# Optimization experiments

Hardware: AMD Instinct MI355X
Metric: run time of the kernel (lower is better)

Reference implementation:

```python
import jax, jax.numpy as jnp
import numpy as np

D_MODEL = 1024
H = 16
D_HEAD = D_MODEL // H
MASK_VAL = -1e30


def setup_inputs() -> dict:
    key = jax.random.key(0)
    ks = jax.random.split(key, 10)
    B, S = 2, 2048
    scale = 1.0 / np.sqrt(D_MODEL)
    return {
        "query": jax.random.normal(ks[0], (B, S, D_MODEL), jnp.float32),
        "key": jax.random.normal(ks[1], (B, S, D_MODEL), jnp.float32),
        "value": jax.random.normal(ks[2], (B, S, D_MODEL), jnp.float32),
        "mask": jax.random.randint(ks[3], (B, S, S), 0, 2) > 0,
        "Wq": jax.random.normal(ks[4], (D_MODEL, D_MODEL), jnp.float32) * scale,
        "bq": jnp.zeros((D_MODEL,), jnp.float32),
        "Wk": jax.random.normal(ks[5], (D_MODEL, D_MODEL), jnp.float32) * scale,
        "bk": jnp.zeros((D_MODEL,), jnp.float32),
        "Wv": jax.random.normal(ks[6], (D_MODEL, D_MODEL), jnp.float32) * scale,
        "bv": jnp.zeros((D_MODEL,), jnp.float32),
    }


def _split_heads(x, B, S):
    # [B,S,D] -> [B,H,S,Dh]
    return x.reshape(B, S, H, D_HEAD).transpose(0, 2, 1, 3)


def reference(query, key, value, mask, Wq, bq, Wk, bk, Wv, bv):
    B, S, _ = query.shape
    q = _split_heads(query @ Wq.T + bq, B, S)
    k = _split_heads(key @ Wk.T + bk, B, S)
    v = _split_heads(value @ Wv.T + bv, B, S)
    # scale by sqrt of per-head dim (query.size(-1) after split)
    q = q / jnp.sqrt(jnp.asarray(D_HEAD, q.dtype))
    scores = jnp.einsum("bhqd,bhkd->bhqk", q, k)
    scores = jnp.where(mask[:, None, :, :], MASK_VAL, scores)
    attn = jax.nn.softmax(scores, axis=-1)
    out = jnp.einsum("bhqk,bhkd->bhqd", attn, v)
    return out.transpose(0, 2, 1, 3).reshape(B, S, D_MODEL)
```

## Files before the change

### kernel.cpp

```cpp
#include <hip/hip_runtime.h>
#include <hip/hip_bf16.h>

#define D_MODEL 1024
#define NH 16
#define DH 64
#define S_LEN 2048
#define BATCH 2
#define QSCALE (0.125f * 1.44269504088896f)

#define KV_HSTRIDE (S_LEN * DH)
#define WS_V_OFF   (NH * KV_HSTRIDE)
#define KVB_WORDS  (2 * NH * KV_HSTRIDE)
#define MB_WORDS   ((S_LEN / 64) * S_LEN)
#define KTILE 128
#define NT (S_LEN / KTILE)
#define X_ELEMS (BATCH * S_LEN * D_MODEL)
#define W_ELEMS (D_MODEL * D_MODEL)
#define KSTR 88
#define VSTR 136
#define BUFW (128 * KSTR + 64 * VSTR)
#define BUF_BYTES (BUFW * 2)

typedef __attribute__((ext_vector_type(8))) short bf16x8;
typedef __attribute__((ext_vector_type(4))) float f32x4;
typedef __attribute__((ext_vector_type(2))) unsigned int u32x2;

static __device__ inline unsigned short f2bf(float f) {
    union { float f; unsigned u; } v; v.f = f;
    unsigned r = v.u + 0x7fffu + ((v.u >> 16) & 1u);
    return (unsigned short)(r >> 16);
}
static __device__ inline unsigned cvt2(float a, float b) {
    union { __hip_bfloat162 h2; unsigned u; } cv;
    cv.h2 = __float22bfloat162_rn(make_float2(a, b));
    return cv.u;
}
static __device__ inline bf16x8 pack8(f32x4 a, f32x4 b) {
    union { bf16x8 v; unsigned u[4]; } r;
    r.u[0] = cvt2(a[0], a[1]); r.u[1] = cvt2(a[2], a[3]);
    r.u[2] = cvt2(b[0], b[1]); r.u[3] = cvt2(b[2], b[3]);
    return r.v;
}
static __device__ inline bf16x8 cvt8(const float* __restrict__ p) {
    return pack8(*(const f32x4*)p, *(const f32x4*)(p + 4));
}
static __device__ inline float exp2_fast(float x) {
#if __has_builtin(__builtin_amdgcn_exp2f)
    return __builtin_amdgcn_exp2f(x);
#else
    return exp2f(x);
#endif
}
static __device__ inline void gload_lds16(const unsigned short* __restrict__ g,
                                          unsigned short* l, int lane) {
#if __has_builtin(__builtin_amdgcn_global_load_lds)
    __builtin_amdgcn_global_load_lds(
        (const __attribute__((address_space(1))) void*)g,
        (__attribute__((address_space(3))) void*)l, 16, 0, 0);
#else
    *(bf16x8*)((char*)l + lane * 16) = *(const bf16x8*)g;
#endif
}
static __device__ inline int vperm(int s) {
    return (s & ~31) | ((s & 12) << 1) | ((s & 16) >> 2) | (s & 3);
}

__global__ __launch_bounds__(256) void cvt_kernel(
    const float* __restrict__ q, const float* __restrict__ k,
    const float* __restrict__ v,
    const float* __restrict__ Wq, const float* __restrict__ Wk,
    const float* __restrict__ Wv,
    unsigned short* __restrict__ xb, unsigned short* __restrict__ wb)
{
    const int by = blockIdx.y;
    const float* src;
    unsigned short* dst;
    size_t base;
    if (blockIdx.x < 1024) {
        src = by == 0 ? q : (by == 1 ? k : v);
        dst = xb + (size_t)by * X_ELEMS;
        base = (size_t)blockIdx.x * 4096;
    } else {
        src = by == 0 ? Wq : (by == 1 ? Wk : Wv);
        dst = wb + (size_t)by * W_ELEMS;
        base = (size_t)(blockIdx.x - 1024) * 4096;
    }
    const int tid = threadIdx.x;
#pragma unroll
    for (int j = 0; j < 4; ++j) {
        const size_t o = base + (size_t)j * 1024 + (size_t)tid * 4;
        const f32x4 a = *(const f32x4*)(src + o);
        u32x2 r;
        r[0] = cvt2(a[0], a[1]);
        r[1] = cvt2(a[2], a[3]);
        *(u32x2*)&dst[o] = r;
    }
}

__global__ __launch_bounds__(256) void pack_mask_kernel(
    const int* __restrict__ mask, unsigned long long* __restrict__ mbits,
    int b_base)
{
    const int w    = blockIdx.x * 4 + (threadIdx.x >> 6);
    const int lane = threadIdx.x & 63;
    const int b    = b_base + (w >> 16);
    const int rem  = w & 65535;
    const int kt   = rem >> 11;
    const int s    = rem & 2047;
    const int v = mask[((size_t)b * S_LEN + s) * S_LEN + kt * 64 + lane];
    const unsigned long long bits = __ballot(v != 0);
    if (lane == 0) mbits[w] = bits;
}

__global__ __launch_bounds__(256) void proj_v2_kernel(
    const unsigned short* __restrict__ xb, const unsigned short* __restrict__ wb,
    const float* __restrict__ bq, const float* __restrict__ bk,
    const float* __restrict__ bv,
    float* __restrict__ q_out, unsigned short* __restrict__ ws)
{
    const int bx = blockIdx.x;
    const int by = blockIdx.y;
    const int z  = by >> 3;
    const int c0 = (by & 7) * 128;

    const unsigned short* A  = xb + (size_t)z * X_ELEMS;
    const unsigned short* Bw = wb + (size_t)z * W_ELEMS;
    const float* bias = z == 0 ? bq : (z == 1 ? bk : bv);

    const int tid  = threadIdx.x;
    const int wave = tid >> 6;
    const int lane = tid & 63;
    const int quad = lane >> 4;
    const int l16  = lane & 15;
    const int m0   = (wave & 1) * 64;
    const int n0   = (wave >> 1) * 64;

    __shared__ __align__(16) unsigned short As[128 * 32];
    __shared__ __align__(16) unsigned short Bs[128 * 32];

    const int r_lo = wave * 16 + (lane >> 2);
    const int r_hi = (wave + 4) * 16 + (lane >> 2);
    const int segu = (lane & 3) * 8;
    const int row0 = bx * 128;

    f32x4 acc[4][4] = {};

    for (int kk = 0; kk < D_MODEL; kk += 32) {
        gload_lds16(A  + (size_t)(row0 + r_lo) * D_MODEL + kk + segu, &As[wave * 512], lane);
        gload_lds16(A  + (size_t)(row0 + r_hi) * D_MODEL + kk + segu, &As[(wave + 4) * 512], lane);
        gload_lds16(Bw + (size_t)(c0 + r_lo) * D_MODEL + kk + segu, &Bs[wave * 512], lane);
        gload_lds16(Bw + (size_t)(c0 + r_hi) * D_MODEL + kk + segu, &Bs[(wave + 4) * 512], lane);
        __syncthreads();

        bf16x8 af[4], bfr[4];
#pragma unroll
        for (int i = 0; i < 4; ++i)
            af[i] = *(const bf16x8*)&As[(m0 + i * 16 + l16) * 32 + quad * 8];
#pragma unroll
        for (int j = 0; j < 4; ++j)
            bfr[j] = *(const bf16x8*)&Bs[(n0 + j * 16 + l16) * 32 + quad * 8];
#pragma unroll
        for (int i = 0; i < 4; ++i)
#pragma unroll
            for (int j = 0; j < 4; ++j)
                acc[i][j] = __builtin_amdgcn_mfma_f32_16x16x32_bf16(
                    af[i], bfr[j], acc[i][j], 0, 0, 0);
        __syncthreads();
    }

#pragma unroll
    for (int j = 0; j < 4; ++j) {
        const int cl  = c0 + n0 + j * 16 + l16;
        const float bval = bias[cl];
        const int h  = cl >> 6;
        const int dh = cl & 63;
#pragma unroll
        for (int i = 0; i < 4; ++i) {
#pragma unroll
            for (int r = 0; r < 4; ++r) {
                const int row = row0 + m0 + i * 16 + quad * 4 + r;
                const float v = acc[i][j][r] + bval;
                if (z == 0) {
                    q_out[(size_t)row * D_MODEL + cl] = v * QSCALE;
                } else {
                    unsigned short* slab = ws + (size_t)(row >> 11) * KVB_WORDS;
                    const int s = row & 2047;
                    if (z == 1)
                        slab[(size_t)h * KV_HSTRIDE + s * DH + dh] = f2bf(v);
                    else
                        slab[WS_V_OFF + (size_t)h * KV_HSTRIDE + dh * S_LEN + vperm(s)] = f2bf(v);
                }
            }
        }
    }
}

__global__ __launch_bounds__(256) void proj_fb_kernel(
    const float* __restrict__ q_in, const float* __restrict__ k_in,
    const float* __restrict__ v_in,
    const float* __restrict__ Wq, const float* __restrict__ bq,
    const float* __restrict__ Wk, const float* __restrict__ bk,
    const float* __restrict__ Wv, const float* __restrict__ bv,
    float* __restrict__ q_out, unsigned short* __restrict__ ws, int b_base)
{
    const int bx = blockIdx.x;
    const int by = blockIdx.y;
    const int z  = by >> 3;
    const int c0 = (by & 7) * 128;

    const float* x    = z == 0 ? q_in : (z == 1 ? k_in : v_in);
    const float* W    = z == 0 ? Wq   : (z == 1 ? Wk   : Wv);
    const float* bias = z == 0 ? bq   : (z == 1 ? bk   : bv);

    const int tid  = threadIdx.x;
    const int wave = tid >> 6;
    const int lane = tid & 63;
    const int quad = lane >> 4;
    const int l16  = lane & 15;
    const int m0   = (wave & 1) * 64;
    const int n0   = (wave >> 1) * 64;

    __shared__ __align__(16) unsigned short As[128][40];
    __shared__ __align__(16) unsigned short Bs[128][40];

    const int srow = tid >> 1;
    const int kcol = (tid & 1) * 16;
    const int row0 = b_base * S_LEN + bx * 128;
    const float* ag = x + (size_t)(row0 + srow) * D_MODEL + kcol;
    const float* bg = W + (size_t)(c0 + srow) * D_MODEL + kcol;

    f32x4 acc[4][4] = {};

    for (int kk = 0; kk < D_MODEL; kk += 32) {
        {
            f32x4 a0 = *(const f32x4*)(ag + kk);
            f32x4 a1 = *(const f32x4*)(ag + kk + 4);
            f32x4 a2 = *(const f32x4*)(ag + kk + 8);
            f32x4 a3 = *(const f32x4*)(ag + kk + 12);
            f32x4 b0 = *(const f32x4*)(bg + kk);
            f32x4 b1 = *(const f32x4*)(bg + kk + 4);
            f32x4 b2 = *(const f32x4*)(bg + kk + 8);
            f32x4 b3 = *(const f32x4*)(bg + kk + 12);
            *(bf16x8*)&As[srow][kcol]     = pack8(a0, a1);
            *(bf16x8*)&As[srow][kcol + 8] = pack8(a2, a3);
            *(bf16x8*)&Bs[srow][kcol]     = pack8(b0, b1);
            *(bf16x8*)&Bs[srow][kcol + 8] = pack8(b2, b3);
        }
        __syncthreads();

        bf16x8 af[4], bfr[4];
#pragma unroll
        for (int i = 0; i < 4; ++i)
            af[i] = *(const bf16x8*)&As[m0 + i * 16 + l16][quad * 8];
#pragma unroll
        for (int j = 0; j < 4; ++j)
            bfr[j] = *(const bf16x8*)&Bs[n0 + j * 16 + l16][quad * 8];
#pragma unroll
        for (int i = 0; i < 4; ++i)
#pragma unroll
            for (int j = 0; j < 4; ++j)
                acc[i][j] = __builtin_amdgcn_mfma_f32_16x16x32_bf16(
                    af[i], bfr[j], acc[i][j], 0, 0, 0);
        __syncthreads();
    }

#pragma unroll
    for (int j = 0; j < 4; ++j) {
        const int cl  = c0 + n0 + j * 16 + l16;
        const float bval = bias[cl];
        const int h  = cl >> 6;
        const int dh = cl & 63;
#pragma unroll
        for (int i = 0; i < 4; ++i) {
#pragma unroll
            for (int r = 0; r < 4; ++r) {
                const int row = row0 + m0 + i * 16 + quad * 4 + r;
                const float v = acc[i][j][r] + bval;
                if (z == 0) {
                    q_out[(size_t)row * D_MODEL + cl] = v * QSCALE;
                } else {
                    const int b_rel = (row >> 11) - b_base;
                    const int s     = row & 2047;
                    unsigned short* slab = ws + (size_t)b_rel * KVB_WORDS;
                    if (z == 1)
                        slab[(size_t)h * KV_HSTRIDE + s * DH + dh] = f2bf(v);
                    else
                        slab[WS_V_OFF + (size_t)h * KV_HSTRIDE + dh * S_LEN + vperm(s)] = f2bf(v);
                }
            }
        }
    }
}

__global__ __launch_bounds__(256) void attn_db_kernel(
    const unsigned short* __restrict__ ws,
    const unsigned long long* __restrict__ mbits,
    float* __restrict__ out)
{
    const int h     = blockIdx.x;
    const int qtile = blockIdx.y;
    const int bz    = blockIdx.z;

    const unsigned short* K  = ws + (size_t)bz * KVB_WORDS + (size_t)h * KV_HSTRIDE;
    const unsigned short* Vg = K + WS_V_OFF;
    const unsigned long long* mb = mbits + (size_t)bz * MB_WORDS;

    const int tid  = threadIdx.x;
    const int wave = tid >> 6;
    const int lane = tid & 63;
    const int quad = lane >> 4;
    const int l16  = lane & 15;
    const int q0   = qtile * 128;

    extern __shared__ __align__(16) unsigned short lds[];

    bf16x8 aq0a, aq1a, aq0b, aq1b;
    {
        const float* qa =
            out + (size_t)(bz * S_LEN + q0 + wave * 16 + l16) * D_MODEL + h * DH;
        const float* qb = qa + (size_t)64 * D_MODEL;
        aq0a = cvt8(qa + quad * 8);  aq1a = cvt8(qa + 32 + quad * 8);
        aq0b = cvt8(qb + quad * 8);  aq1b = cvt8(qb + 32 + quad * 8);
    }

    bf16x8 ones;
    {
        union { bf16x8 v; unsigned short u[8]; } o;
#pragma unroll
        for (int i = 0; i < 8; ++i) o.u[i] = 0x3F80;
        ones = o.v;
    }

    const int qg = q0 + wave * 16 + l16;
    f32x4 l_acc_a = {0.f, 0.f, 0.f, 0.f};
    f32x4 l_acc_b = {0.f, 0.f, 0.f, 0.f};
    f32x4 o_a[4] = {}, o_b[4] = {};

    const int krow = tid >> 1, kc = (tid & 1) * 32;
    const int vrow = tid >> 2, vc = (tid & 3) * 32;
    bf16x8 kr[4], vr[4];
    {
        const unsigned short* kp = K + (size_t)krow * DH + kc;
        const unsigned short* vp = Vg + (size_t)vrow * S_LEN + vc;
#pragma unroll
        for (int i = 0; i < 4; ++i) {
            kr[i] = *(const bf16x8*)(kp + 8 * i);
            vr[i] = *(const bf16x8*)(vp + 8 * i);
        }
    }
    unsigned long long wm0a = mb[qg] >> (quad * 4);
    unsigned long long wm1a = mb[(size_t)S_LEN + qg] >> (quad * 4);
    unsigned long long wm0b = mb[qg + 64] >> (quad * 4);
    unsigned long long wm1b = mb[(size_t)S_LEN + qg + 64] >> (quad * 4);

    {
        unsigned short* Kt0 = lds;
        unsigned short* Vt0 = lds + 128 * KSTR;
#pragma unroll
        for (int i = 0; i < 4; ++i) {
            *(bf16x8*)&Kt0[krow * KSTR + kc + 8 * i] = kr[i];
            *(bf16x8*)&Vt0[vrow * VSTR + vc + 8 * i] = vr[i];
        }
    }

    for (int kt = 0; kt < NT; ++kt) {
        __syncthreads();
        unsigned short* Ktc = lds + (kt & 1) * BUFW;
        unsigned short* Vtc = Ktc + 128 * KSTR;

        if (kt + 1 < NT) {
            const unsigned short* kp = K + (size_t)((kt + 1) * KTILE + krow) * DH + kc;
            const unsigned short* vp = Vg + (size_t)vrow * S_LEN + (kt + 1) * KTILE + vc;
#pragma unroll
            for (int i = 0; i < 4; ++i) {
                kr[i] = *(const bf16x8*)(kp + 8 * i);
                vr[i] = *(const bf16x8*)(vp + 8 * i);
            }
        }
        unsigned long long nm0a = 0ull, nm1a = 0ull, nm0b = 0ull, nm1b = 0ull;
        if (kt + 1 < NT) {
            nm0a = mb[(size_t)(2 * kt + 2) * S_LEN + qg] >> (quad * 4);
            nm1a = mb[(size_t)(2 * kt + 3) * S_LEN + qg] >> (quad * 4);
            nm0b = mb[(size_t)(2 * kt + 2) * S_LEN + qg + 64] >> (quad * 4);
            nm1b = mb[(size_t)(2 * kt + 3) * S_LEN + qg + 64] >> (quad * 4);
        }

        bf16x8 af_a[4], af_b[4];
#pragma unroll
        for (int c = 0; c < 4; ++c) {
            f32x4 sa[2], sb[2];
            __builtin_amdgcn_s_setprio(1);
#pragma unroll
            for (int j = 0; j < 2; ++j) {
                const int blk = 2 * c + j;
                const unsigned short* kb = &Ktc[(blk * 16 + l16) * KSTR];
                bf16x8 k0 = *(const bf16x8*)&kb[quad * 8];
                bf16x8 k1 = *(const bf16x8*)&kb[32 + quad * 8];
                f32x4 z = {0.f, 0.f, 0.f, 0.f};
                sa[j] = __builtin_amdgcn_mfma_f32_16x16x32_bf16(k0, aq0a, z, 0, 0, 0);
                sa[j] = __builtin_amdgcn_mfma_f32_16x16x32_bf16(k1, aq1a, sa[j], 0, 0, 0);
                sb[j] = __builtin_amdgcn_mfma_f32_16x16x32_bf16(k0, aq0b, z, 0, 0, 0);
                sb[j] = __builtin_amdgcn_mfma_f32_16x16x32_bf16(k1, aq1b, sb[j], 0, 0, 0);
            }
            __builtin_amdgcn_s_setprio(0);
#pragma unroll
            for (int j = 0; j < 2; ++j) {
                const int blk = 2 * c + j;
                const unsigned long long wa = (blk < 4) ? wm0a : wm1a;
                const unsigned long long wb = (blk < 4) ? wm0b : wm1b;
                const int sh = (blk & 3) * 16;
#pragma unroll
                for (int r = 0; r < 4; ++r) {
                    const bool ma  = (wa >> (sh + r)) & 1ull;
                    const bool mbk = (wb >> (sh + r)) & 1ull;
                    sa[j][r] = ma  ? 0.0f : exp2_fast(sa[j][r]);
                    sb[j][r] = mbk ? 0.0f : exp2_fast(sb[j][r]);
                }
            }
            {
                union { bf16x8 v; unsigned u[4]; } pk;
                pk.u[0] = cvt2(sa[0][0], sa[0][1]);
                pk.u[1] = cvt2(sa[0][2], sa[0][3]);
                pk.u[2] = cvt2(sa[1][0], sa[1][1]);
                pk.u[3] = cvt2(sa[1][2], sa[1][3]);
                af_a[c] = pk.v;
                pk.u[0] = cvt2(sb[0][0], sb[0][1]);
                pk.u[1] = cvt2(sb[0][2], sb[0][3]);
                pk.u[2] = cvt2(sb[1][0], sb[1][1]);
                pk.u[3] = cvt2(sb[1][2], sb[1][3]);
                af_b[c] = pk.v;
            }
        }

        __builtin_amdgcn_s_setprio(1);
#pragma unroll
        for (int c = 0; c < 4; ++c) {
            l_acc_a = __builtin_amdgcn_mfma_f32_16x16x32_bf16(af_a[c], ones, l_acc_a, 0, 0, 0);
            l_acc_b = __builtin_amdgcn_mfma_f32_16x16x32_bf16(af_b[c], ones, l_acc_b, 0, 0, 0);
        }
#pragma unroll
        for (int d = 0; d < 4; ++d) {
#pragma unroll
            for (int c = 0; c < 4; ++c) {
                bf16x8 bv = *(const bf16x8*)&Vtc[(d * 16 + l16) * VSTR + c * 32 + quad * 8];
                o_a[d] = __builtin_amdgcn_mfma_f32_16x16x32_bf16(af_a[c], bv, o_a[d], 0, 0, 0);
                o_b[d] = __builtin_amdgcn_mfma_f32_16x16x32_bf16(af_b[c], bv, o_b[d], 0, 0, 0);
            }
        }
        __builtin_amdgcn_s_setprio(0);

        if (kt + 1 < NT) {
            unsigned short* Ktn = lds + ((kt + 1) & 1) * BUFW;
            unsigned short* Vtn = Ktn + 128 * KSTR;
#pragma unroll
            for (int i = 0; i < 4; ++i) {
                *(bf16x8*)&Ktn[krow * KSTR + kc + 8 * i] = kr[i];
                *(bf16x8*)&Vtn[vrow * VSTR + vc + 8 * i] = vr[i];
            }
        }
        wm0a = nm0a; wm1a = nm1a; wm0b = nm0b; wm1b = nm1b;
    }

#pragma unroll
    for (int r = 0; r < 4; ++r) {
        const float ia = 1.0f / fmaxf(l_acc_a[r], 1e-30f);
        const float ib = 1.0f / fmaxf(l_acc_b[r], 1e-30f);
        const int qgr = q0 + wave * 16 + quad * 4 + r;
#pragma unroll
        for (int d = 0; d < 4; ++d) {
            out[((size_t)(bz * S_LEN) + qgr) * D_MODEL + h * DH + d * 16 + l16] =
                o_a[d][r] * ia;
            out[((size_t)(bz * S_LEN) + qgr + 64) * D_MODEL + h * DH + d * 16 + l16] =
                o_b[d][r] * ib;
        }
    }
}

__global__ __launch_bounds__(256) void attn_sb_kernel(
    const unsigned short* __restrict__ ws,
    const unsigned long long* __restrict__ mbits,
    const int* __restrict__ mask,
    float* __restrict__ out, int b_base, int use_bits)
{
    const int h     = blockIdx.x;
    const int qtile = blockIdx.y;
    const int bz    = blockIdx.z;
    const int b0    = b_base + bz;

    const unsigned short* K  = ws + (size_t)bz * KVB_WORDS + (size_t)h * KV_HSTRIDE;
    const unsigned short* Vg = K + WS_V_OFF;
    const unsigned long long* mb = mbits + (size_t)bz * MB_WORDS;

    const int tid  = threadIdx.x;
    const int wave = tid >> 6;
    const int lane = tid & 63;
    const int quad = lane >> 4;
    const int l16  = lane & 15;
    const int q0   = qtile * 128;

    __shared__ __align__(16) unsigned short Vt[64][VSTR];
    __shared__ __align__(16) unsigned short Kt[128 * KSTR];

    bf16x8 aq0a, aq1a, aq0b, aq1b;
    {
        const float* qa =
            out + (size_t)(b0 * S_LEN + q0 + wave * 16 + l16) * D_MODEL + h * DH;
        const float* qb = qa + (size_t)64 * D_MODEL;
        aq0a = cvt8(qa + quad * 8);  aq1a = cvt8(qa + 32 + quad * 8);
        aq0b = cvt8(qb + quad * 8);  aq1b = cvt8(qb + 32 + quad * 8);
    }

    const int qg = q0 + wave * 16 + l16;
    float l_a = 0.f, l_b = 0.f;
    f32x4 o_a[4] = {}, o_b[4] = {};

    const int krow = tid >> 1, kc = (tid & 1) * 32;
    const int vrow = tid >> 2, vc = (tid & 3) * 32;
    bf16x8 kr[4], vr[4];
    {
        const unsigned short* kp = K + (size_t)krow * DH + kc;
        const unsigned short* vp = Vg + (size_t)vrow * S_LEN + vc;
#pragma unroll
        for (int i = 0; i < 4; ++i) {
            kr[i] = *(const bf16x8*)(kp + 8 * i);
            vr[i] = *(const bf16x8*)(vp + 8 * i);
        }
    }

    for (int kt = 0; kt < NT; ++kt) {
#pragma unroll
        for (int i = 0; i < 4; ++i) {
            *(bf16x8*)&Kt[krow * KSTR + kc + 8 * i] = kr[i];
            *(bf16x8*)&Vt[vrow][vc + 8 * i]         = vr[i];
        }
        __syncthreads();

        if (kt + 1 < NT) {
            const unsigned short* kp = K + (size_t)((kt + 1) * KTILE + krow) * DH + kc;
            const unsigned short* vp = Vg + (size_t)vrow * S_LEN + (kt + 1) * KTILE + vc;
#pragma unroll
            for (int i = 0; i < 4; ++i) {
                kr[i] = *(const bf16x8*)(kp + 8 * i);
                vr[i] = *(const bf16x8*)(vp + 8 * i);
            }
        }

        unsigned long long wm0a = 0ull, wm1a = 0ull, wm0b = 0ull, wm1b = 0ull;
        if (use_bits) {
            wm0a = mb[(size_t)(2 * kt) * S_LEN + qg] >> (quad * 4);
            wm1a = mb[(size_t)(2 * kt + 1) * S_LEN + qg] >> (quad * 4);
            wm0b = mb[(size_t)(2 * kt) * S_LEN + qg + 64] >> (quad * 4);
            wm1b = mb[(size_t)(2 * kt + 1) * S_LEN + qg + 64] >> (quad * 4);
        }

        bf16x8 af_a[4], af_b[4];
#pragma unroll
        for (int c = 0; c < 4; ++c) {
            f32x4 sa[2], sb[2];
#pragma unroll
            for (int j = 0; j < 2; ++j) {
                const int blk = 2 * c + j;
                const unsigned short* kb = &Kt[(blk * 16 + l16) * KSTR];
                bf16x8 k0 = *(const bf16x8*)&kb[quad * 8];
                bf16x8 k1 = *(const bf16x8*)&kb[32 + quad * 8];
                f32x4 z = {0.f, 0.f, 0.f, 0.f};
                sa[j] = __builtin_amdgcn_mfma_f32_16x16x32_bf16(k0, aq0a, z, 0, 0, 0);
                sa[j] = __builtin_amdgcn_mfma_f32_16x16x32_bf16(k1, aq1a, sa[j], 0, 0, 0);
                sb[j] = __builtin_amdgcn_mfma_f32_16x16x32_bf16(k0, aq0b, z, 0, 0, 0);
                sb[j] = __builtin_amdgcn_mfma_f32_16x16x32_bf16(k1, aq1b, sb[j], 0, 0, 0);
            }
#pragma unroll
            for (int j = 0; j < 2; ++j) {
                const int blk = 2 * c + j;
                const unsigned long long wa = (blk < 4) ? wm0a : wm1a;
                const unsigned long long wb = (blk < 4) ? wm0b : wm1b;
                const int sh = (blk & 3) * 16;
#pragma unroll
                for (int r = 0; r < 4; ++r) {
                    bool ma, mbk;
                    if (use_bits) {
                        ma  = (wa >> (sh + r)) & 1ull;
                        mbk = (wb >> (sh + r)) & 1ull;
                    } else {
                        const int kg = kt * KTILE + blk * 16 + quad * 4 + r;
                        ma  = mask[((size_t)(b0 * S_LEN) + qg) * S_LEN + kg] != 0;
                        mbk = mask[((size_t)(b0 * S_LEN) + qg + 64) * S_LEN + kg] != 0;
                    }
                    const float pa = ma  ? 0.0f : exp2_fast(sa[j][r]);
                    const float pb = mbk ? 0.0f : exp2_fast(sb[j][r]);
                    sa[j][r] = pa; l_a += pa;
                    sb[j][r] = pb; l_b += pb;
                }
            }
            {
                union { bf16x8 v; unsigned u[4]; } pk;
                pk.u[0] = cvt2(sa[0][0], sa[0][1]);
                pk.u[1] = cvt2(sa[0][2], sa[0][3]);
                pk.u[2] = cvt2(sa[1][0], sa[1][1]);
                pk.u[3] = cvt2(sa[1][2], sa[1][3]);
                af_a[c] = pk.v;
                pk.u[0] = cvt2(sb[0][0], sb[0][1]);
                pk.u[1] = cvt2(sb[0][2], sb[0][3]);
                pk.u[2] = cvt2(sb[1][0], sb[1][1]);
                pk.u[3] = cvt2(sb[1][2], sb[1][3]);
                af_b[c] = pk.v;
            }
        }

#pragma unroll
        for (int d = 0; d < 4; ++d) {
#pragma unroll
            for (int c = 0; c < 4; ++c) {
                bf16x8 bv = *(const bf16x8*)&Vt[d * 16 + l16][c * 32 + quad * 8];
                o_a[d] = __builtin_amdgcn_mfma_f32_16x16x32_bf16(af_a[c], bv, o_a[d], 0, 0, 0);
                o_b[d] = __builtin_amdgcn_mfma_f32_16x16x32_bf16(af_b[c], bv, o_b[d], 0, 0, 0);
            }
        }
        __syncthreads();
    }

    l_a += __shfl_xor(l_a, 16, 64);
    l_a += __shfl_xor(l_a, 32, 64);
    l_b += __shfl_xor(l_b, 16, 64);
    l_b += __shfl_xor(l_b, 32, 64);

#pragma unroll
    for (int r = 0; r < 4; ++r) {
        const float la = __shfl(l_a, quad * 4 + r, 64);
        const float lb = __shfl(l_b, quad * 4 + r, 64);
        const float ia = 1.0f / fmaxf(la, 1e-30f);
        const float ib = 1.0f / fmaxf(lb, 1e-30f);
        const int qgr = q0 + wave * 16 + quad * 4 + r;
#pragma unroll
        for (int d = 0; d < 4; ++d) {
            out[((size_t)(b0 * S_LEN) + qgr) * D_MODEL + h * DH + d * 16 + l16] =
                o_a[d][r] * ia;
            out[((size_t)(b0 * S_LEN) + qgr + 64) * D_MODEL + h * DH + d * 16 + l16] =
                o_b[d][r] * ib;
        }
    }
}

extern "C" void kernel_launch(void* const* d_in, const int* in_sizes, int n_in,
                              void* d_out, int out_size, void* d_ws, size_t ws_size,
                              hipStream_t stream) {
    const float* query = (const float*)d_in[0];
    const float* key   = (const float*)d_in[1];
    const float* value = (const float*)d_in[2];
    const int*   mask  = (const int*)d_in[3];
    const float* Wq    = (const float*)d_in[4];
    const float* bq    = (const float*)d_in[5];
    const float* Wk    = (const float*)d_in[6];
    const float* bk    = (const float*)d_in[7];
    const float* Wv    = (const float*)d_in[8];
    const float* bv    = (const float*)d_in[9];

    unsigned short* ws   = (unsigned short*)d_ws;
    float*          outp = (float*)d_out;

    const size_t KV_BYTES = (size_t)KVB_WORDS * 2;
    const size_t MB_BYTES = (size_t)MB_WORDS * 8;
    const size_t XB_BYTES = (size_t)3 * X_ELEMS * 2;
    const size_t WB_BYTES = (size_t)3 * W_ELEMS * 2;
    const size_t base2    = 2 * KV_BYTES + 2 * MB_BYTES;

    static int db_ok = -1;
    if (db_ok < 0) {
        hipError_t e = hipFuncSetAttribute(
            reinterpret_cast<const void*>(attn_db_kernel),
            hipFuncAttributeMaxDynamicSharedMemorySize, 2 * BUF_BYTES);
        db_ok = (e == hipSuccess) ? 1 : 0;
    }

    if (ws_size >= base2 + XB_BYTES + WB_BYTES) {
        unsigned long long* mbits = (unsigned long long*)(ws + 2 * KVB_WORDS);
        unsigned short* xb = ws + base2 / 2;
        unsigned short* wb = xb + (size_t)3 * X_ELEMS;
        cvt_kernel<<<dim3(1280, 3), 256, 0, stream>>>(
            query, key, value, Wq, Wk, Wv, xb, wb);
        proj_v2_kernel<<<dim3(32, 24), 256, 0, stream>>>(
            xb, wb, bq, bk, bv, outp, ws);
        pack_mask_kernel<<<dim3(2 * MB_WORDS / 4), 256, 0, stream>>>(mask, mbits, 0);
        if (db_ok)
            attn_db_kernel<<<dim3(NH, S_LEN / 128, 2), 256, 2 * BUF_BYTES, stream>>>(
                ws, mbits, outp);
        else
            attn_sb_kernel<<<dim3(NH, S_LEN / 128, 2), 256, 0, stream>>>(
                ws, mbits, mask, outp, 0, 1);
    } else if (ws_size >= base2) {
        unsigned long long* mbits = (unsigned long long*)(ws + 2 * KVB_WORDS);
        proj_fb_kernel<<<dim3(32, 24), 256, 0, stream>>>(
            query, key, value, Wq, bq, Wk, bk, Wv, bv, outp, ws, 0);
        pack_mask_kernel<<<dim3(2 * MB_WORDS / 4), 256, 0, stream>>>(mask, mbits, 0);
        if (db_ok)
            attn_db_kernel<<<dim3(NH, S_LEN / 128, 2), 256, 2 * BUF_BYTES, stream>>>(
                ws, mbits, outp);
        else
            attn_sb_kernel<<<dim3(NH, S_LEN / 128, 2), 256, 0, stream>>>(
                ws, mbits, mask, outp, 0, 1);
    } else if (ws_size >= KV_BYTES + MB_BYTES) {
        unsigned long long* mbits = (unsigned long long*)(ws + KVB_WORDS);
        for (int b0 = 0; b0 < BATCH; ++b0) {
            proj_fb_kernel<<<dim3(16, 24), 256, 0, stream>>>(
                query, key, value, Wq, bq, Wk, bk, Wv, bv, outp, ws, b0);
            pack_mask_kernel<<<dim3(MB_WORDS / 4), 256, 0, stream>>>(mask, mbits, b0);
            attn_sb_kernel<<<dim3(NH, S_LEN / 128, 1), 256, 0, stream>>>(
                ws, mbits, mask, outp, b0, 1);
        }
    } else {
        for (int b0 = 0; b0 < BATCH; ++b0) {
            proj_fb_kernel<<<dim3(16, 24), 256, 0, stream>>>(
                query, key, value, Wq, bq, Wk, bk, Wv, bv, outp, ws, b0);
            attn_sb_kernel<<<dim3(NH, S_LEN / 128, 1), 256, 0, stream>>>(
                ws, (const unsigned long long*)ws, mask, outp, b0, 0);
        }
    }
}
```

Before: 252.6 us.

## Load V fragments directly from global memory and sum softmax denominators on VALU

The attention kernel stops staging V tiles in shared memory. Each wave now reads its V MFMA operands straight from global memory (the transposed V layout), and only K is double-buffered in static LDS. The row-sum of probabilities is accumulated with scalar adds plus cross-lane shuffles instead of extra MFMAs against a ones vector, and the dynamic-LDS attribute setup is removed. This shrinks LDS use and LDS traffic and may raise occupancy. The cost is that every wave redundantly fetches the same V data from global/L2, and the V loads sit on the critical path with less latency hiding.

```diff
diff --git a/kernel.cpp b/kernel.cpp
--- a/kernel.cpp
+++ b/kernel.cpp
@@ -18,8 +18,6 @@
 #define W_ELEMS (D_MODEL * D_MODEL)
 #define KSTR 88
 #define VSTR 136
-#define BUFW (128 * KSTR + 64 * VSTR)
-#define BUF_BYTES (BUFW * 2)
 
 typedef __attribute__((ext_vector_type(8))) short bf16x8;
 typedef __attribute__((ext_vector_type(4))) float f32x4;
@@ -312,7 +310,7 @@
     const int l16  = lane & 15;
     const int q0   = qtile * 128;
 
-    extern __shared__ __align__(16) unsigned short lds[];
+    __shared__ __align__(16) unsigned short Kt[2][128 * KSTR];
 
     bf16x8 aq0a, aq1a, aq0b, aq1b;
     {
@@ -323,59 +321,43 @@
         aq0b = cvt8(qb + quad * 8);  aq1b = cvt8(qb + 32 + quad * 8);
     }
 
-    bf16x8 ones;
-    {
-        union { bf16x8 v; unsigned short u[8]; } o;
-#pragma unroll
-        for (int i = 0; i < 8; ++i) o.u[i] = 0x3F80;
-        ones = o.v;
-    }
-
     const int qg = q0 + wave * 16 + l16;
-    f32x4 l_acc_a = {0.f, 0.f, 0.f, 0.f};
-    f32x4 l_acc_b = {0.f, 0.f, 0.f, 0.f};
+    float l_a = 0.f, l_b = 0.f;
     f32x4 o_a[4] = {}, o_b[4] = {};
 
     const int krow = tid >> 1, kc = (tid & 1) * 32;
-    const int vrow = tid >> 2, vc = (tid & 3) * 32;
-    bf16x8 kr[4], vr[4];
+    bf16x8 kr[4];
     {
         const unsigned short* kp = K + (size_t)krow * DH + kc;
-        const unsigned short* vp = Vg + (size_t)vrow * S_LEN + vc;
-#pragma unroll
-        for (int i = 0; i < 4; ++i) {
-            kr[i] = *(const bf16x8*)(kp + 8 * i);
-            vr[i] = *(const bf16x8*)(vp + 8 * i);
-        }
-    }
+#pragma unroll
+        for (int i = 0; i < 4; ++i) kr[i] = *(const bf16x8*)(kp + 8 * i);
+    }
+    const unsigned short* vbase = Vg + (size_t)l16 * S_LEN + quad * 8;
+
     unsigned long long wm0a = mb[qg] >> (quad * 4);
     unsigned long long wm1a = mb[(size_t)S_LEN + qg] >> (quad * 4);
     unsigned long long wm0b = mb[qg + 64] >> (quad * 4);
     unsigned long long wm1b = mb[(size_t)S_LEN + qg + 64] >> (quad * 4);
 
-    {
-        unsigned short* Kt0 = lds;
-        unsigned short* Vt0 = lds + 128 * KSTR;
-#pragma unroll
-        for (int i = 0; i < 4; ++i) {
-            *(bf16x8*)&Kt0[krow * KSTR + kc + 8 * i] = kr[i];
-            *(bf16x8*)&Vt0[vrow * VSTR + vc + 8 * i] = vr[i];
-        }
-    }
+#pragma unroll
+    for (int i = 0; i < 4; ++i)
+        *(bf16x8*)&Kt[0][krow * KSTR + kc + 8 * i] = kr[i];
 
     for (int kt = 0; kt < NT; ++kt) {
         __syncthreads();
-        unsigned short* Ktc = lds + (kt & 1) * BUFW;
-        unsigned short* Vtc = Ktc + 128 * KSTR;
+        const unsigned short* Ktc = Kt[kt & 1];
+        const unsigned short* vcol = vbase + kt * KTILE;
 
         if (kt + 1 < NT) {
             const unsigned short* kp = K + (size_t)((kt + 1) * KTILE + krow) * DH + kc;
-            const unsigned short* vp = Vg + (size_t)vrow * S_LEN + (kt + 1) * KTILE + vc;
-#pragma unroll
-            for (int i = 0; i < 4; ++i) {
-                kr[i] = *(const bf16x8*)(kp + 8 * i);
-                vr[i] = *(const bf16x8*)(vp + 8 * i);
-            }
+#pragma unroll
+            for (int i = 0; i < 4; ++i) kr[i] = *(const bf16x8*)(kp + 8 * i);
+        }
+        bf16x8 vA0[4], vA1[4];
+#pragma unroll
+        for (int c = 0; c < 4; ++c) {
+            vA0[c] = *(const bf16x8*)(vcol + c * 32);
+            vA1[c] = *(const bf16x8*)(vcol + (size_t)16 * S_LEN + c * 32);
         }
         unsigned long long nm0a = 0ull, nm1a = 0ull, nm0b = 0ull, nm1b = 0ull;
         if (kt + 1 < NT) {
@@ -385,86 +367,102 @@
             nm1b = mb[(size_t)(2 * kt + 3) * S_LEN + qg + 64] >> (quad * 4);
         }
 
+        f32x4 sa[8], sb[8];
+        __builtin_amdgcn_s_setprio(1);
+#pragma unroll
+        for (int blk = 0; blk < 8; ++blk) {
+            const unsigned short* kb = &Ktc[(blk * 16 + l16) * KSTR];
+            bf16x8 k0 = *(const bf16x8*)&kb[quad * 8];
+            bf16x8 k1 = *(const bf16x8*)&kb[32 + quad * 8];
+            f32x4 z = {0.f, 0.f, 0.f, 0.f};
+            sa[blk] = __builtin_amdgcn_mfma_f32_16x16x32_bf16(k0, aq0a, z, 0, 0, 0);
+            sa[blk] = __builtin_amdgcn_mfma_f32_16x16x32_bf16(k1, aq1a, sa[blk], 0, 0, 0);
+            sb[blk] = __builtin_amdgcn_mfma_f32_16x16x32_bf16(k0, aq0b, z, 0, 0, 0);
+            sb[blk] = __builtin_amdgcn_mfma_f32_16x16x32_bf16(k1, aq1b, sb[blk], 0, 0, 0);
+        }
+        __builtin_amdgcn_s_setprio(0);
+
+        bf16x8 vB0[4], vB1[4];
+#pragma unroll
+        for (int c = 0; c < 4; ++c) {
+            vB0[c] = *(const bf16x8*)(vcol + (size_t)32 * S_LEN + c * 32);
+            vB1[c] = *(const bf16x8*)(vcol + (size_t)48 * S_LEN + c * 32);
+        }
+
+#pragma unroll
+        for (int blk = 0; blk < 8; ++blk) {
+            const unsigned long long wa = (blk < 4) ? wm0a : wm1a;
+            const unsigned long long wb = (blk < 4) ? wm0b : wm1b;
+            const int sh = (blk & 3) * 16;
+#pragma unroll
+            for (int r = 0; r < 4; ++r) {
+                const bool ma  = (wa >> (sh + r)) & 1ull;
+                const bool mbk = (wb >> (sh + r)) & 1ull;
+                const float pa = ma  ? 0.0f : exp2_fast(sa[blk][r]);
+                const float pb = mbk ? 0.0f : exp2_fast(sb[blk][r]);
+                sa[blk][r] = pa; l_a += pa;
+                sb[blk][r] = pb; l_b += pb;
+            }
+        }
+
         bf16x8 af_a[4], af_b[4];
 #pragma unroll
         for (int c = 0; c < 4; ++c) {
-            f32x4 sa[2], sb[2];
-            __builtin_amdgcn_s_setprio(1);
-#pragma unroll
-            for (int j = 0; j < 2; ++j) {
-                const int blk = 2 * c + j;
-                const unsigned short* kb = &Ktc[(blk * 16 + l16) * KSTR];
-                bf16x8 k0 = *(const bf16x8*)&kb[quad * 8];
-                bf16x8 k1 = *(const bf16x8*)&kb[32 + quad * 8];
-                f32x4 z = {0.f, 0.f, 0.f, 0.f};
-                sa[j] = __builtin_amdgcn_mfma_f32_16x16x32_bf16(k0, aq0a, z, 0, 0, 0);
-                sa[j] = __builtin_amdgcn_mfma_f32_16x16x32_bf16(k1, aq1a, sa[j], 0, 0, 0);
-                sb[j] = __builtin_amdgcn_mfma_f32_16x16x32_bf16(k0, aq0b, z, 0, 0, 0);
-                sb[j] = __builtin_amdgcn_mfma_f32_16x16x32_bf16(k1, aq1b, sb[j], 0, 0, 0);
-            }
-            __builtin_amdgcn_s_setprio(0);
-#pragma unroll
-            for (int j = 0; j < 2; ++j) {
-                const int blk = 2 * c + j;
-                const unsigned long long wa = (blk < 4) ? wm0a : wm1a;
-                const unsigned long long wb = (blk < 4) ? wm0b : wm1b;
-                const int sh = (blk & 3) * 16;
-#pragma unroll
-                for (int r = 0; r < 4; ++r) {
-                    const bool ma  = (wa >> (sh + r)) & 1ull;
-                    const bool mbk = (wb >> (sh + r)) & 1ull;
-                    sa[j][r] = ma  ? 0.0f : exp2_fast(sa[j][r]);
-                    sb[j][r] = mbk ? 0.0f : exp2_fast(sb[j][r]);
-                }
-            }
-            {
-                union { bf16x8 v; unsigned u[4]; } pk;
-                pk.u[0] = cvt2(sa[0][0], sa[0][1]);
-                pk.u[1] = cvt2(sa[0][2], sa[0][3]);
-                pk.u[2] = cvt2(sa[1][0], sa[1][1]);
-                pk.u[3] = cvt2(sa[1][2], sa[1][3]);
-                af_a[c] = pk.v;
-                pk.u[0] = cvt2(sb[0][0], sb[0][1]);
-                pk.u[1] = cvt2(sb[0][2], sb[0][3]);
-                pk.u[2] = cvt2(sb[1][0], sb[1][1]);
-                pk.u[3] = cvt2(sb[1][2], sb[1][3]);
-                af_b[c] = pk.v;
-            }
+            union { bf16x8 v; unsigned u[4]; } pk;
+            pk.u[0] = cvt2(sa[2 * c][0],     sa[2 * c][1]);
+            pk.u[1] = cvt2(sa[2 * c][2],     sa[2 * c][3]);
+            pk.u[2] = cvt2(sa[2 * c + 1][0], sa[2 * c + 1][1]);
+            pk.u[3] = cvt2(sa[2 * c + 1][2], sa[2 * c + 1][3]);
+            af_a[c] = pk.v;
+            pk.u[0] = cvt2(sb[2 * c][0],     sb[2 * c][1]);
+            pk.u[1] = cvt2(sb[2 * c][2],     sb[2 * c][3]);
+            pk.u[2] = cvt2(sb[2 * c + 1][0], sb[2 * c + 1][1]);
+            pk.u[3] = cvt2(sb[2 * c + 1][2], sb[2 * c + 1][3]);
+            af_b[c] = pk.v;
         }
 
         __builtin_amdgcn_s_setprio(1);
 #pragma unroll
         for (int c = 0; c < 4; ++c) {
-            l_acc_a = __builtin_amdgcn_mfma_f32_16x16x32_bf16(af_a[c], ones, l_acc_a, 0, 0, 0);
-            l_acc_b = __builtin_amdgcn_mfma_f32_16x16x32_bf16(af_b[c], ones, l_acc_b, 0, 0, 0);
-        }
-#pragma unroll
-        for (int d = 0; d < 4; ++d) {
-#pragma unroll
-            for (int c = 0; c < 4; ++c) {
-                bf16x8 bv = *(const bf16x8*)&Vtc[(d * 16 + l16) * VSTR + c * 32 + quad * 8];
-                o_a[d] = __builtin_amdgcn_mfma_f32_16x16x32_bf16(af_a[c], bv, o_a[d], 0, 0, 0);
-                o_b[d] = __builtin_amdgcn_mfma_f32_16x16x32_bf16(af_b[c], bv, o_b[d], 0, 0, 0);
-            }
+            o_a[0] = __builtin_amdgcn_mfma_f32_16x16x32_bf16(af_a[c], vA0[c], o_a[0], 0, 0, 0);
+            o_b[0] = __builtin_amdgcn_mfma_f32_16x16x32_bf16(af_b[c], vA0[c], o_b[0], 0, 0, 0);
+        }
+#pragma unroll
+        for (int c = 0; c < 4; ++c) {
+            o_a[1] = __builtin_amdgcn_mfma_f32_16x16x32_bf16(af_a[c], vA1[c], o_a[1], 0, 0, 0);
+            o_b[1] = __builtin_amdgcn_mfma_f32_16x16x32_bf16(af_b[c], vA1[c], o_b[1], 0, 0, 0);
+        }
+#pragma unroll
+        for (int c = 0; c < 4; ++c) {
+            o_a[2] = __builtin_amdgcn_mfma_f32_16x16x32_bf16(af_a[c], vB0[c], o_a[2], 0, 0, 0);
+            o_b[2] = __builtin_amdgcn_mfma_f32_16x16x32_bf16(af_b[c], vB0[c], o_b[2], 0, 0, 0);
+        }
+#pragma unroll
+        for (int c = 0; c < 4; ++c) {
+            o_a[3] = __builtin_amdgcn_mfma_f32_16x16x32_bf16(af_a[c], vB1[c], o_a[3], 0, 0, 0);
+            o_b[3] = __builtin_amdgcn_mfma_f32_16x16x32_bf16(af_b[c], vB1[c], o_b[3], 0, 0, 0);
         }
         __builtin_amdgcn_s_setprio(0);
 
         if (kt + 1 < NT) {
-            unsigned short* Ktn = lds + ((kt + 1) & 1) * BUFW;
-            unsigned short* Vtn = Ktn + 128 * KSTR;
-#pragma unroll
-            for (int i = 0; i < 4; ++i) {
-                *(bf16x8*)&Ktn[krow * KSTR + kc + 8 * i] = kr[i];
-                *(bf16x8*)&Vtn[vrow * VSTR + vc + 8 * i] = vr[i];
-            }
+#pragma unroll
+            for (int i = 0; i < 4; ++i)
+                *(bf16x8*)&Kt[(kt + 1) & 1][krow * KSTR + kc + 8 * i] = kr[i];
         }
         wm0a = nm0a; wm1a = nm1a; wm0b = nm0b; wm1b = nm1b;
     }
 
+    l_a += __shfl_xor(l_a, 16, 64);
+    l_a += __shfl_xor(l_a, 32, 64);
+    l_b += __shfl_xor(l_b, 16, 64);
+    l_b += __shfl_xor(l_b, 32, 64);
+
 #pragma unroll
     for (int r = 0; r < 4; ++r) {
-        const float ia = 1.0f / fmaxf(l_acc_a[r], 1e-30f);
-        const float ib = 1.0f / fmaxf(l_acc_b[r], 1e-30f);
+        const float la = __shfl(l_a, quad * 4 + r, 64);
+        const float lb = __shfl(l_b, quad * 4 + r, 64);
+        const float ia = 1.0f / fmaxf(la, 1e-30f);
+        const float ib = 1.0f / fmaxf(lb, 1e-30f);
         const int qgr = q0 + wave * 16 + quad * 4 + r;
 #pragma unroll
         for (int d = 0; d < 4; ++d) {
@@ -664,14 +662,6 @@
     const size_t WB_BYTES = (size_t)3 * W_ELEMS * 2;
     const size_t base2    = 2 * KV_BYTES + 2 * MB_BYTES;
 
-    static int db_ok = -1;
-    if (db_ok < 0) {
-        hipError_t e = hipFuncSetAttribute(
-            reinterpret_cast<const void*>(attn_db_kernel),
-            hipFuncAttributeMaxDynamicSharedMemorySize, 2 * BUF_BYTES);
-        db_ok = (e == hipSuccess) ? 1 : 0;
-    }
-
     if (ws_size >= base2 + XB_BYTES + WB_BYTES) {
         unsigned long long* mbits = (unsigned long long*)(ws + 2 * KVB_WORDS);
         unsigned short* xb = ws + base2 / 2;
@@ -681,23 +671,15 @@
         proj_v2_kernel<<<dim3(32, 24), 256, 0, stream>>>(
             xb, wb, bq, bk, bv, outp, ws);
         pack_mask_kernel<<<dim3(2 * MB_WORDS / 4), 256, 0, stream>>>(mask, mbits, 0);
-        if (db_ok)
-            attn_db_kernel<<<dim3(NH, S_LEN / 128, 2), 256, 2 * BUF_BYTES, stream>>>(
-                ws, mbits, outp);
-        else
-            attn_sb_kernel<<<dim3(NH, S_LEN / 128, 2), 256, 0, stream>>>(
-                ws, mbits, mask, outp, 0, 1);
+        attn_db_kernel<<<dim3(NH, S_LEN / 128, 2), 256, 0, stream>>>(
+            ws, mbits, outp);
     } else if (ws_size >= base2) {
         unsigned long long* mbits = (unsigned long long*)(ws + 2 * KVB_WORDS);
         proj_fb_kernel<<<dim3(32, 24), 256, 0, stream>>>(
             query, key, value, Wq, bq, Wk, bk, Wv, bv, outp, ws, 0);
         pack_mask_kernel<<<dim3(2 * MB_WORDS / 4), 256, 0, stream>>>(mask, mbits, 0);
-        if (db_ok)
-            attn_db_kernel<<<dim3(NH, S_LEN / 128, 2), 256, 2 * BUF_BYTES, stream>>>(
-                ws, mbits, outp);
-        else
-            attn_sb_kernel<<<dim3(NH, S_LEN / 128, 2), 256, 0, stream>>>(
-                ws, mbits, mask, outp, 0, 1);
+        attn_db_kernel<<<dim3(NH, S_LEN / 128, 2), 256, 0, stream>>>(
+            ws, mbits, outp);
     } else if (ws_size >= KV_BYTES + MB_BYTES) {
         unsigned long long* mbits = (unsigned long long*)(ws + KVB_WORDS);
         for (int b0 = 0; b0 < BATCH; ++b0) {
```

Measured after the change: 298.3 us. 1.18x slower.
